# Kernel optimization log

Hardware: AMD Instinct MI355X
Metric: run time of the kernel (lower is better)

## Reference

```python
import jax, jax.numpy as jnp
import numpy as np

N, E, C, H, T, R = 32768, 262144, 128, 8, 8, 8
DK = C // H


def _typed_linear(feat, W, b, tid):
    # per-type linear: rows with tid==t get feat @ W[t] + b[t]; others untouched base 0
    out = jnp.zeros((feat.shape[0], W.shape[-1]), feat.dtype)
    for t in range(W.shape[0]):
        m = (tid == t)[:, None]
        out = jnp.where(m, feat @ W[t] + b[t], out)
    return out


def _forward(x, type_id, edge_index, edge_attr, Wk, bk, Wq, bq, Wv, bv, Wa, ba,
             relation_pri, relation_att, relation_msg, skip, gamma, beta):
    n, c = x.shape
    r, h, dk, _ = relation_att.shape
    src, dst = edge_index[0], edge_index[1]
    fs, fd = x[src], x[dst]                      # [E, C] gathers
    # per-edge-type k/q/v projections (source masks by edge_attr)
    k = _typed_linear(fs, Wk, bk, edge_attr).reshape(-1, h, dk)
    q = _typed_linear(fd, Wq, bq, edge_attr).reshape(-1, h, dk)
    v = _typed_linear(fs, Wv, bv, edge_attr).reshape(-1, h, dk)
    # relation transforms without materializing [E,h,dk,dk] gathers
    kt = jnp.zeros_like(k)
    vt = jnp.zeros_like(v)
    for ri in range(r):
        m = (edge_attr == ri)[:, None, None]
        kt = jnp.where(m, jnp.einsum('ehd,hdk->ehk', k, relation_att[ri]), kt)
        vt = jnp.where(m, jnp.einsum('ehd,hdk->ehk', v, relation_msg[ri]), vt)
    pri = relation_pri[edge_attr]                # [E, H]
    att = (q * kt).sum(-1) * pri / jnp.sqrt(jnp.asarray(dk, x.dtype))  # [E, H]
    # scatter softmax over destination-node groups
    mx = jax.ops.segment_max(att, dst, num_segments=n)
    ex = jnp.exp(att - mx[dst])
    den = jax.ops.segment_sum(ex, dst, num_segments=n)
    a = ex / den[dst]                            # [E, H]
    w = (a[..., None] * vt).reshape(-1, h * dk)  # [E, C]
    # scatter mean into node slots (zeros for isolated nodes)
    s = jax.ops.segment_sum(w, dst, num_segments=n)
    cnt = jax.ops.segment_sum(jnp.ones((w.shape[0], 1), x.dtype), dst, num_segments=n)
    x0 = jnp.where(cnt > 0, s / jnp.maximum(cnt, 1.0), 0.0)
    # per-node-type output projection + gated residual
    x0 = _typed_linear(x0, Wa, ba, type_id)
    alpha = jax.nn.sigmoid(skip)[type_id][:, None]
    out = x0 * alpha + x * (1.0 - alpha)
    # type-indexed LayerNorm (eps = 1e-5), dropout is identity in eval
    mu = out.mean(-1, keepdims=True)
    var = ((out - mu) ** 2).mean(-1, keepdims=True)
    xn = (out - mu) / jnp.sqrt(var + 1e-5)
    return xn * gamma[type_id] + beta[type_id]


def setup_inputs() -> dict:
    key = jax.random.key(0)
    ks = jax.random.split(key, 16)
    w = 1.0 / np.sqrt(C)
    wr = 1.0 / np.sqrt(DK)
    return {
        'x': jax.random.normal(ks[0], (N, C), jnp.float32),
        'type_id': jax.random.randint(ks[1], (N,), 0, T),
        'edge_index': jax.random.randint(ks[2], (2, E), 0, N),
        'edge_attr': jax.random.randint(ks[3], (E,), 0, R),
        'Wk': jax.random.normal(ks[4], (T, C, C), jnp.float32) * w,
        'bk': jax.random.normal(ks[5], (T, C), jnp.float32) * 0.02,
        'Wq': jax.random.normal(ks[6], (T, C, C), jnp.float32) * w,
        'bq': jax.random.normal(ks[7], (T, C), jnp.float32) * 0.02,
        'Wv': jax.random.normal(ks[8], (T, C, C), jnp.float32) * w,
        'bv': jax.random.normal(ks[9], (T, C), jnp.float32) * 0.02,
        'Wa': jax.random.normal(ks[10], (T, C, C), jnp.float32) * w,
        'ba': jax.random.normal(ks[11], (T, C), jnp.float32) * 0.02,
        'relation_pri': jnp.ones((R, H), jnp.float32),
        'relation_att': jax.random.normal(ks[12], (R, H, DK, DK), jnp.float32) * wr,
        'relation_msg': jax.random.normal(ks[13], (R, H, DK, DK), jnp.float32) * wr,
        'skip': jnp.ones((T,), jnp.float32),
        'gamma': jnp.ones((T, C), jnp.float32),
        'beta': jnp.zeros((T, C), jnp.float32),
    }


def reference(x, type_id, edge_index, edge_attr, Wk, bk, Wq, bq, Wv, bv, Wa, ba,
              relation_pri, relation_att, relation_msg, skip, gamma, beta):
    return _forward(x, type_id, edge_index, edge_attr, Wk, bk, Wq, bq, Wv, bv, Wa, ba,
                    relation_pri, relation_att, relation_msg, skip, gamma, beta)
```

## Files before the change

### kernel.cpp

```cpp
#include <hip/hip_runtime.h>
#include <math.h>

#define NN 32768
#define NE 262144
#define CD 128
#define NH 8
#define NT 8
#define NR 8

typedef unsigned short u16;
typedef unsigned long long ull;
typedef __attribute__((ext_vector_type(8))) short bhalf8;
typedef __attribute__((ext_vector_type(4))) float f32x4;


__device__ __forceinline__ u16 f2b(float f) {
    union { float f; unsigned u; } v; v.f = f;
    unsigned r = v.u + 0x7FFF + ((v.u >> 16) & 1);
    return (u16)(r >> 16);
}
__device__ __forceinline__ float b2f(unsigned h) {
    union { unsigned u; float f; } v; v.u = h << 16;
    return v.f;
}

#define PREP_BLOCKS 2057
#define XB_BLOCKS 2048
#define HIST_BLOCKS 1024

__global__ void prep_all(const float* __restrict__ Wk, const float* __restrict__ bk,
                         const float* __restrict__ Wq,
                         const float* __restrict__ Wv, const float* __restrict__ bv,
                         const float* __restrict__ Wa,
                         const float* __restrict__ Aatt, const float* __restrict__ Amsg,
                         const float* __restrict__ x,
                         const int* __restrict__ ea, const int* __restrict__ tidv,
                         const int* __restrict__ dstv,
                         u16* __restrict__ WqT, u16* __restrict__ WkT,
                         u16* __restrict__ WvT, u16* __restrict__ WaT,
                         float* __restrict__ bkf, float* __restrict__ bvf,
                         u16* __restrict__ xb,
                         int* __restrict__ epart, int* __restrict__ npart,
                         int* __restrict__ deg) {
    const int bx = blockIdx.x;
    if (bx >= PREP_BLOCKS + XB_BLOCKS) {
        __shared__ int wc[4][8];
        const int hb = bx - PREP_BLOCKS - XB_BLOCKS;
        const int tid = threadIdx.x;
        const int lane = tid & 63, w = tid >> 6;
        int i = hb * 256 + tid;
        int t = ea[i];
        atomicAdd(&deg[dstv[i]], 1);
#pragma unroll
        for (int u = 0; u < 8; ++u) {
            ull m = __ballot(t == u);
            if (lane == 0) wc[w][u] = __popcll(m);
        }
        __syncthreads();
        if (tid < 8) epart[hb * 8 + tid] = wc[0][tid] + wc[1][tid] + wc[2][tid] + wc[3][tid];
        if (hb < NN / 256) {
            int tn = tidv[i];
            __syncthreads();
#pragma unroll
            for (int u = 0; u < 8; ++u) {
                ull m = __ballot(tn == u);
                if (lane == 0) wc[w][u] = __popcll(m);
            }
            __syncthreads();
            if (tid < 8) npart[hb * 8 + tid] = wc[0][tid] + wc[1][tid] + wc[2][tid] + wc[3][tid];
        }
        return;
    }
    if (bx >= PREP_BLOCKS) {
        int zi = (bx - PREP_BLOCKS) * 256 + threadIdx.x;
        long basei = (long)zi * 8;
        float4 v0 = *(const float4*)(x + basei);
        float4 v1 = *(const float4*)(x + basei + 4);
        bhalf8 pk;
        pk[0] = (short)f2b(v0.x); pk[1] = (short)f2b(v0.y);
        pk[2] = (short)f2b(v0.z); pk[3] = (short)f2b(v0.w);
        pk[4] = (short)f2b(v1.x); pk[5] = (short)f2b(v1.y);
        pk[6] = (short)f2b(v1.z); pk[7] = (short)f2b(v1.w);
        *(bhalf8*)(xb + basei) = pk;
        return;
    }
    const int WCNT = NT * CD * CD;
    int idx = bx * 256 + threadIdx.x;
    if (idx < 4 * WCNT) {
        int mat = idx >> 17;
        int o = idx & (WCNT - 1);
        int t = o >> 14;
        int n = (o >> 7) & 127;
        int k = o & 127;
        int ct = n >> 4, lx2 = n & 15, kk = k >> 5, qd = (k >> 3) & 3, dd = k & 7;
        int oo = t * 16384 + (((ct * 4 + kk) * 4 + qd) * 16 + lx2) * 8 + dd;
        if (mat == 0) {
            WqT[oo] = f2b(Wq[(t * CD + k) * CD + n]);
        } else if (mat == 3) {
            WaT[oo] = f2b(Wa[(t * CD + k) * CD + n]);
        } else {
            int h = n >> 4, j = n & 15;
            const float* W = (mat == 1) ? Wk : Wv;
            const float* A = (mat == 1) ? Aatt : Amsg;
            const float* wrow = W + (t * CD + k) * CD + h * 16;
            const float* acol = A + ((t * NH + h) * 16) * 16 + j;
            float s = 0.f;
#pragma unroll
            for (int d = 0; d < 16; ++d) s += wrow[d] * acol[d * 16];
            ((mat == 1) ? WkT : WvT)[oo] = f2b(s);
        }
    } else {
        int o2 = idx - 4 * WCNT;
        if (o2 < 2 * NT * CD) {
            int which = (o2 >= NT * CD) ? 1 : 0;
            int o = o2 - which * NT * CD;
            const float* B = which ? bv : bk;
            const float* A = which ? Amsg : Aatt;
            int t = o >> 7; int c = o & 127; int h = c >> 4; int j = c & 15;
            const float* brow = B + t * CD + h * 16;
            const float* acol = A + ((t * NH + h) * 16) * 16 + j;
            float s = 0.f;
#pragma unroll
            for (int d = 0; d < 16; ++d) s += brow[d] * acol[d * 16];
            (which ? bvf : bkf)[o] = s;
        }
    }
}

__launch_bounds__(1024)
__global__ void scan_all(const int* __restrict__ deg, int* __restrict__ dbase,
                         int* __restrict__ epart, int* __restrict__ npart,
                         int* __restrict__ ectr, int* __restrict__ nctr) {
    const int t = threadIdx.x;
    if (blockIdx.x == 0) {
        __shared__ int part[1024];
        int local[32];
        int s = 0;
#pragma unroll
        for (int i = 0; i < 32; ++i) { local[i] = s; s += deg[t * 32 + i]; }
        part[t] = s;
        __syncthreads();
        for (int off = 1; off < 1024; off <<= 1) {
            int v = (t >= off) ? part[t - off] : 0;
            __syncthreads();
            part[t] += v;
            __syncthreads();
        }
        int base = (t == 0) ? 0 : part[t - 1];
#pragma unroll
        for (int i = 0; i < 32; ++i) dbase[t * 32 + i] = base + local[i];
        return;
    }
    __shared__ int sc[1024 * 8];
    int v[8], orig[8];
#pragma unroll
    for (int u = 0; u < 8; ++u) { orig[u] = v[u] = epart[t * 8 + u]; sc[t * 8 + u] = v[u]; }
    for (int off = 1; off < 1024; off <<= 1) {
        __syncthreads();
        int wv[8];
        bool p = (t >= off);
        if (p) {
#pragma unroll
            for (int u = 0; u < 8; ++u) wv[u] = sc[(t - off) * 8 + u];
        }
        __syncthreads();
        if (p) {
#pragma unroll
            for (int u = 0; u < 8; ++u) { v[u] += wv[u]; sc[t * 8 + u] = v[u]; }
        }
    }
    __syncthreads();
    int tot[8], base[8];
    {
        int acc = 0;
#pragma unroll
        for (int u = 0; u < 8; ++u) { tot[u] = sc[1023 * 8 + u]; base[u] = acc; acc += tot[u]; }
    }
#pragma unroll
    for (int u = 0; u < 8; ++u) epart[t * 8 + u] = base[u] + v[u] - orig[u];
    if (t == 0) {
        ectr[8] = 0; ectr[17] = 0;
        int acc = 0, ptb = 0;
        for (int u = 0; u < 8; ++u) {
            acc += tot[u]; ectr[9 + u] = acc;
            ptb += (tot[u] + 63) >> 6; ectr[18 + u] = ptb;
        }
    }
    __syncthreads();
    int nv[8], nor[8];
#pragma unroll
    for (int u = 0; u < 8; ++u) {
        nor[u] = nv[u] = (t < 128) ? npart[t * 8 + u] : 0;
        sc[t * 8 + u] = nv[u];
    }
    for (int off = 1; off < 128; off <<= 1) {
        __syncthreads();
        int wv[8];
        bool p = (t >= off && t < 128);
        if (p) {
#pragma unroll
            for (int u = 0; u < 8; ++u) wv[u] = sc[(t - off) * 8 + u];
        }
        __syncthreads();
        if (p) {
#pragma unroll
            for (int u = 0; u < 8; ++u) { nv[u] += wv[u]; sc[t * 8 + u] = nv[u]; }
        }
    }
    __syncthreads();
    int ntot[8], nbase[8];
    {
        int acc = 0;
#pragma unroll
        for (int u = 0; u < 8; ++u) { ntot[u] = sc[127 * 8 + u]; nbase[u] = acc; acc += ntot[u]; }
    }
    if (t < 128) {
#pragma unroll
        for (int u = 0; u < 8; ++u) npart[t * 8 + u] = nbase[u] + nv[u] - nor[u];
    }
    if (t == 0) {
        nctr[8] = 0; nctr[17] = 0;
        int acc = 0, ptb = 0;
        for (int u = 0; u < 8; ++u) {
            acc += ntot[u]; nctr[9 + u] = acc;
            ptb += (ntot[u] + 63) >> 6; nctr[18 + u] = ptb;
        }
    }
}

__global__ void scatter2(const int* __restrict__ ea, const int* __restrict__ tidv,
                         const int* __restrict__ srcv, const int* __restrict__ dstv,
                         const int* __restrict__ epart, const int* __restrict__ npart,
                         const int* __restrict__ dbase, int* __restrict__ dcur,
                         int4* __restrict__ epack, int* __restrict__ nperm) {
    __shared__ int wc[4][8];
    __shared__ int wo[4][8];
    const int b = blockIdx.x;
    const int tid = threadIdx.x;
    const int lane = tid & 63, w = tid >> 6;
    const bool is_e = (b < NE / 256);
    const int* lab; const int* off; int i;
    if (is_e) { lab = ea; off = epart + b * 8; i = b * 256 + tid; }
    else { lab = tidv; off = npart + (b - NE / 256) * 8; i = (b - NE / 256) * 256 + tid; }
    int t = lab[i];
    const ull below = (1ull << lane) - 1;
    int myrank = 0;
#pragma unroll
    for (int u = 0; u < 8; ++u) {
        ull m = __ballot(t == u);
        if (lane == 0) wc[w][u] = __popcll(m);
        if (t == u) myrank = __popcll(m & below);
    }
    __syncthreads();
    if (tid < 32) {
        int u = tid & 7, w2 = tid >> 3;
        int s = 0;
        for (int w3 = 0; w3 < w2; ++w3) s += wc[w3][u];
        wo[w2][u] = s;
    }
    __syncthreads();
    int slot = off[t] + wo[w][t] + myrank;
    if (is_e) {
        int s = srcv[i], d = dstv[i];
        int pos = dbase[d] + atomicAdd(&dcur[d], 1);
        epack[slot] = int4{s, d, pos, 0};
    } else {
        nperm[slot] = i;
    }
}

__device__ __forceinline__ void gemm64g(const u16* __restrict__ sA,
                                        const u16* __restrict__ gW,
                                        int rh, int ch, int lx, int quad, int lane,
                                        const float* __restrict__ biasRow,
                                        f32x4 acc[2][4]) {
#pragma unroll
    for (int nt = 0; nt < 4; ++nt) {
        float bv = biasRow[ch * 64 + nt * 16 + lx];
        acc[0][nt] = f32x4{bv, bv, bv, bv};
        acc[1][nt] = f32x4{bv, bv, bv, bv};
    }
    const int m0 = rh * 32 + lx;
    const u16* wbase = gW + (ch * 4) * 2048 + lane * 8;
    bhalf8 bb[2][4];
#pragma unroll
    for (int nt = 0; nt < 4; ++nt)
        bb[0][nt] = *(const bhalf8*)(wbase + nt * 2048);
#pragma unroll
    for (int kk = 0; kk < 4; ++kk) {
        if (kk < 3) {
#pragma unroll
            for (int nt = 0; nt < 4; ++nt)
                bb[(kk + 1) & 1][nt] = *(const bhalf8*)(wbase + nt * 2048 + (kk + 1) * 512);
        }
        const int ko = kk * 32 + quad * 8;
        bhalf8 a0 = *(const bhalf8*)&sA[m0 * 136 + ko];
        bhalf8 a1 = *(const bhalf8*)&sA[(m0 + 16) * 136 + ko];
#pragma unroll
        for (int nt = 0; nt < 4; ++nt) {
            acc[0][nt] = __builtin_amdgcn_mfma_f32_16x16x32_bf16(a0, bb[kk & 1][nt], acc[0][nt], 0, 0, 0);
            acc[1][nt] = __builtin_amdgcn_mfma_f32_16x16x32_bf16(a1, bb[kk & 1][nt], acc[1][nt], 0, 0, 0);
        }
    }
}

__launch_bounds__(256, 4)
__global__ void edge_kernel(const u16* __restrict__ xb,
                            const u16* __restrict__ WqT, const float* __restrict__ bq,
                            const u16* __restrict__ WkT, const float* __restrict__ bkf,
                            const u16* __restrict__ WvT, const float* __restrict__ bvf,
                            const float* __restrict__ pri,
                            const int* __restrict__ ectr, const int4* __restrict__ epack,
                            float* __restrict__ exs, u16* __restrict__ vts) {
    __shared__ u16 sFS[64 * 136];
    __shared__ u16 sFD[64 * 136];
    __shared__ int sSrc[64], sDst[64], sPos[64];

    const int tid = threadIdx.x;
    const int lane = tid & 63;
    const int w = tid >> 6;
    const int lx = lane & 15;
    const int quad = lane >> 4;
    const int ch = w & 1;
    const int rh = w >> 1;
    const int b = blockIdx.x;

    int t = -1, lt = 0;
#pragma unroll
    for (int u = 0; u < NR; ++u) {
        int p0 = ectr[17 + u], p1 = ectr[18 + u];
        if (b >= p0 && b < p1) { t = u; lt = b - p0; }
    }
    if (t < 0) return;
    const int base = ectr[8 + t];
    const int sz = ectr[9 + t] - base;
    const int start = lt * 64;

    if (tid < 64) {
        int idx = start + tid;
        int4 pk = (idx < sz) ? epack[base + idx] : int4{0, 0, NE, 0};
        sSrc[tid] = pk.x;
        sDst[tid] = pk.y;
        sPos[tid] = pk.z;
    }
    __syncthreads();

#pragma unroll
    for (int it = 0; it < 4; ++it) {
        int c = tid + it * 256;
        int row = c >> 4, off = (c & 15) * 8;
        *(bhalf8*)&sFS[row * 136 + off] = *(const bhalf8*)&xb[(long)sSrc[row] * CD + off];
        *(bhalf8*)&sFD[row * 136 + off] = *(const bhalf8*)&xb[(long)sDst[row] * CD + off];
    }
    __syncthreads();

    f32x4 qa[2][4], ka[2][4];
    gemm64g(sFD, WqT + t * 16384, rh, ch, lx, quad, lane, bq + t * CD, qa);
    gemm64g(sFS, WkT + t * 16384, rh, ch, lx, quad, lane, bkf + t * CD, ka);

    float ex[2][4][4];
#pragma unroll
    for (int nt = 0; nt < 4; ++nt) {
        const float ph = pri[t * NH + ch * 4 + nt] * 0.25f;
#pragma unroll
        for (int mt = 0; mt < 2; ++mt) {
#pragma unroll
            for (int reg = 0; reg < 4; ++reg) {
                float p = qa[mt][nt][reg] * ka[mt][nt][reg];
                p += __shfl_xor(p, 1);
                p += __shfl_xor(p, 2);
                p += __shfl_xor(p, 4);
                p += __shfl_xor(p, 8);
                ex[mt][nt][reg] = __expf(p * ph);
            }
        }
    }
    if (lx == 0) {
#pragma unroll
        for (int mt = 0; mt < 2; ++mt)
#pragma unroll
            for (int reg = 0; reg < 4; ++reg) {
                int erow = rh * 32 + mt * 16 + quad * 4 + reg;
                float4 e4 = {ex[mt][0][reg], ex[mt][1][reg], ex[mt][2][reg], ex[mt][3][reg]};
                *(float4*)(exs + (long)sPos[erow] * 8 + ch * 4) = e4;
            }
    }

    f32x4 va[2][4];
    gemm64g(sFS, WvT + t * 16384, rh, ch, lx, quad, lane, bvf + t * CD, va);
    __syncthreads();
#pragma unroll
    for (int mt = 0; mt < 2; ++mt)
#pragma unroll
        for (int reg = 0; reg < 4; ++reg) {
            int erow = rh * 32 + mt * 16 + quad * 4 + reg;
#pragma unroll
            for (int nt = 0; nt < 4; ++nt)
                sFD[erow * 136 + ch * 64 + nt * 16 + lx] = f2b(va[mt][nt][reg]);
        }
    __syncthreads();
#pragma unroll
    for (int it = 0; it < 4; ++it) {
        int c = tid + it * 256;
        int row = c >> 4, off = (c & 15) * 8;
        *(bhalf8*)&vts[(long)sPos[row] * 128 + off] = *(const bhalf8*)&sFD[row * 136 + off];
    }
}

__launch_bounds__(256, 4)
__global__ void node_kernel(const float* __restrict__ x,
                            const u16* __restrict__ WaT, const float* __restrict__ ba,
                            const float* __restrict__ skip, const float* __restrict__ gamma,
                            const float* __restrict__ beta,
                            const int* __restrict__ nctr, const int* __restrict__ nperm,
                            const int* __restrict__ dbase, const int* __restrict__ deg,
                            const float* __restrict__ exs, const u16* __restrict__ vts,
                            float* __restrict__ out) {
    __shared__ u16 sX0[64 * 136];
    __shared__ int sNode[64], sVal[64];

    const int tid = threadIdx.x;
    const int lane = tid & 63;
    const int w = tid >> 6;
    const int lx = lane & 15;
    const int quad = lane >> 4;
    const int b = blockIdx.x;

    int t = -1, lt = 0;
#pragma unroll
    for (int u = 0; u < NT; ++u) {
        int p0 = nctr[17 + u], p1 = nctr[18 + u];
        if (b >= p0 && b < p1) { t = u; lt = b - p0; }
    }
    if (t < 0) return;
    const int base = nctr[8 + t];
    const int sz = nctr[9 + t] - base;
    const int start = lt * 64;

    if (tid < 64) {
        int idx = start + tid;
        int n = (idx < sz) ? nperm[base + idx] : -1;
        sVal[tid] = (n >= 0) ? 1 : 0;
        sNode[tid] = (n >= 0) ? n : 0;
    }
    __syncthreads();

    {
        const int sub = lane >> 3;
        const int l8 = lane & 7;
        for (int r2 = 0; r2 < 2; ++r2) {
            int row = w * 16 + r2 * 8 + sub;
            int n = sNode[row];
            int s = dbase[n], d = deg[n];
            const u16* vp = vts + (long)s * 128 + l8 * 16;
            const float* ep = exs + (long)s * 8 + l8;
            float aA[16], aB[16];
#pragma unroll
            for (int c = 0; c < 16; ++c) { aA[c] = 0.f; aB[c] = 0.f; }
            float sdA = 0.f, sdB = 0.f;
            int j = 0;
            for (; j + 4 <= d; j += 4) {
                bhalf8 v0a = *(const bhalf8*)(vp + (long)(j + 0) * 128);
                bhalf8 v0b = *(const bhalf8*)(vp + (long)(j + 0) * 128 + 8);
                bhalf8 v1a = *(const bhalf8*)(vp + (long)(j + 1) * 128);
                bhalf8 v1b = *(const bhalf8*)(vp + (long)(j + 1) * 128 + 8);
                bhalf8 v2a = *(const bhalf8*)(vp + (long)(j + 2) * 128);
                bhalf8 v2b = *(const bhalf8*)(vp + (long)(j + 2) * 128 + 8);
                bhalf8 v3a = *(const bhalf8*)(vp + (long)(j + 3) * 128);
                bhalf8 v3b = *(const bhalf8*)(vp + (long)(j + 3) * 128 + 8);
                float e0 = ep[(long)(j + 0) * 8];
                float e1 = ep[(long)(j + 1) * 8];
                float e2 = ep[(long)(j + 2) * 8];
                float e3 = ep[(long)(j + 3) * 8];
#pragma unroll
                for (int c = 0; c < 8; ++c) {
                    aA[c] += e0 * b2f((u16)v0a[c]) + e1 * b2f((u16)v1a[c]);
                    aA[8 + c] += e0 * b2f((u16)v0b[c]) + e1 * b2f((u16)v1b[c]);
                    aB[c] += e2 * b2f((u16)v2a[c]) + e3 * b2f((u16)v3a[c]);
                    aB[8 + c] += e2 * b2f((u16)v2b[c]) + e3 * b2f((u16)v3b[c]);
                }
                sdA += e0 + e1;
                sdB += e2 + e3;
            }
            for (; j < d; ++j) {
                bhalf8 v0a = *(const bhalf8*)(vp + (long)j * 128);
                bhalf8 v0b = *(const bhalf8*)(vp + (long)j * 128 + 8);
                float e0 = ep[(long)j * 8];
#pragma unroll
                for (int c = 0; c < 8; ++c) {
                    aA[c] += e0 * b2f((u16)v0a[c]);
                    aA[8 + c] += e0 * b2f((u16)v0b[c]);
                }
                sdA += e0;
            }
            float sden = sdA + sdB;
            float inv = (d > 0) ? 1.f / (sden * (float)d) : 0.f;
            bhalf8 p0, p1;
#pragma unroll
            for (int c = 0; c < 8; ++c) {
                p0[c] = (short)f2b((aA[c] + aB[c]) * inv);
                p1[c] = (short)f2b((aA[8 + c] + aB[8 + c]) * inv);
            }
            *(bhalf8*)&sX0[row * 136 + l8 * 16] = p0;
            *(bhalf8*)&sX0[row * 136 + l8 * 16 + 8] = p1;
        }
    }
    __syncthreads();

    f32x4 acc[8];
#pragma unroll
    for (int nt = 0; nt < 8; ++nt) {
        float bv = ba[t * CD + nt * 16 + lx];
        acc[nt] = f32x4{bv, bv, bv, bv};
    }
    const int m0 = w * 16 + lx;
    const u16* wbase = WaT + t * 16384 + lane * 8;
#pragma unroll
    for (int kk = 0; kk < 4; ++kk) {
        bhalf8 nb[8];
#pragma unroll
        for (int ct = 0; ct < 8; ++ct)
            nb[ct] = *(const bhalf8*)(wbase + ct * 2048 + kk * 512);
        bhalf8 a = *(const bhalf8*)&sX0[m0 * 136 + kk * 32 + quad * 8];
#pragma unroll
        for (int ct = 0; ct < 8; ++ct)
            acc[ct] = __builtin_amdgcn_mfma_f32_16x16x32_bf16(a, nb[ct], acc[ct], 0, 0, 0);
    }

    const float alpha = 1.f / (1.f + __expf(-skip[t]));
    const float oma = 1.f - alpha;
    float g[8], be[8];
#pragma unroll
    for (int nt = 0; nt < 8; ++nt) {
        g[nt] = gamma[t * CD + nt * 16 + lx];
        be[nt] = beta[t * CD + nt * 16 + lx];
    }
#pragma unroll
    for (int reg = 0; reg < 4; ++reg) {
        int erow = w * 16 + quad * 4 + reg;
        int n = sNode[erow];
        const float* xr = x + (long)n * CD;
        float o[8];
        float s1 = 0.f, s2 = 0.f;
#pragma unroll
        for (int nt = 0; nt < 8; ++nt) {
            float xv = xr[nt * 16 + lx];
            float ov = acc[nt][reg] * alpha + xv * oma;
            o[nt] = ov;
            s1 += ov;
            s2 += ov * ov;
        }
#pragma unroll
        for (int m = 1; m < 16; m <<= 1) {
            s1 += __shfl_xor(s1, m);
            s2 += __shfl_xor(s2, m);
        }
        float mu = s1 * (1.f / 128.f);
        float var = s2 * (1.f / 128.f) - mu * mu;
        float rs = rsqrtf(var + 1e-5f);
        if (sVal[erow]) {
            float* op = out + (long)n * CD;
#pragma unroll
            for (int nt = 0; nt < 8; ++nt)
                __builtin_nontemporal_store((o[nt] - mu) * rs * g[nt] + be[nt],
                                            &op[nt * 16 + lx]);
        }
    }
}

extern "C" void kernel_launch(void* const* d_in, const int* in_sizes, int n_in,
                              void* d_out, int out_size, void* d_ws, size_t ws_size,
                              hipStream_t stream) {
    const float* x        = (const float*)d_in[0];
    const int*   type_id  = (const int*)d_in[1];
    const int*   edge_idx = (const int*)d_in[2];
    const int*   edge_attr= (const int*)d_in[3];
    const float* Wk   = (const float*)d_in[4];
    const float* bk   = (const float*)d_in[5];
    const float* Wq   = (const float*)d_in[6];
    const float* bq   = (const float*)d_in[7];
    const float* Wv   = (const float*)d_in[8];
    const float* bv   = (const float*)d_in[9];
    const float* Wa   = (const float*)d_in[10];
    const float* ba   = (const float*)d_in[11];
    const float* pri  = (const float*)d_in[12];
    const float* Aatt = (const float*)d_in[13];
    const float* Amsg = (const float*)d_in[14];
    const float* skip = (const float*)d_in[15];
    const float* gam  = (const float*)d_in[16];
    const float* bet  = (const float*)d_in[17];

    char* ws = (char*)d_ws;
    u16*   WqT  = (u16*)(ws + 0);
    u16*   WkT  = (u16*)(ws + 262144);
    u16*   WvT  = (u16*)(ws + 524288);
    u16*   WaT  = (u16*)(ws + 786432);
    float* bkf  = (float*)(ws + 1048576);
    float* bvf  = (float*)(ws + 1052672);
    float* exs  = (float*)(ws + 1056768);
    u16*   vts  = (u16*)(ws + 9447424);
    int*   deg  = (int*)  (ws + 76572672);
    int*   dcur = (int*)  (ws + 76703744);
    int*   dbase= (int*)  (ws + 76834816);
    int*   nperm= (int*)  (ws + 78014464);
    int*   ectr = (int*)  (ws + 78145536);
    int*   nctr = (int*)  (ws + 78145792);
    int*   epart= (int*)  (ws + 78146048);
    int*   npart= (int*)  (ws + 78178816);
    u16*   xb   = (u16*)  (ws + 78182912);
    int4*  epack= (int4*) (ws + 86571520);

    const int* src = edge_idx;
    const int* dst = edge_idx + NE;

    hipMemsetAsync(deg, 0, 2 * NN * sizeof(int), stream);
    prep_all<<<PREP_BLOCKS + XB_BLOCKS + HIST_BLOCKS, 256, 0, stream>>>(
        Wk, bk, Wq, Wv, bv, Wa, Aatt, Amsg, x, edge_attr, type_id, dst,
        WqT, WkT, WvT, WaT, bkf, bvf, xb, epart, npart, deg);
    scan_all<<<2, 1024, 0, stream>>>(deg, dbase, epart, npart, ectr, nctr);
    scatter2<<<NE / 256 + NN / 256, 256, 0, stream>>>(edge_attr, type_id, src, dst,
                                                      epart, npart, dbase, dcur,
                                                      epack, nperm);
    edge_kernel<<<NE / 64 + NR, 256, 0, stream>>>(xb, WqT, bq, WkT, bkf, WvT, bvf,
                                                  pri, ectr, epack, exs, vts);
    node_kernel<<<NN / 64 + NT, 256, 0, stream>>>(x, WaT, ba, skip, gam, bet, nctr, nperm,
                                                  dbase, deg, exs, vts, (float*)d_out);
}
```

Measured before the change: 240.8 us.

## Stream dst features directly into Q GEMM registers, drop sFD, use bf16 residual

The edge kernel no longer stages destination-node features in shared memory. The Q projection loads its A operands straight from global bf16 x with register double-buffering, and the V result reuses the sFS buffer. Halving the edge kernel's LDS footprint allows the launch-bounds occupancy hint to rise from 4 to 5 blocks. The node kernel also reads the residual x from the bf16 copy instead of fp32, which halves that traffic but lowers residual precision.

Result: slower. 306.7 us (+27.4%).

```diff
diff --git a/kernel.cpp b/kernel.cpp
--- a/kernel.cpp
+++ b/kernel.cpp
@@ -304,7 +304,7 @@
     }
 }
 
-__launch_bounds__(256, 4)
+__launch_bounds__(256, 5)
 __global__ void edge_kernel(const u16* __restrict__ xb,
                             const u16* __restrict__ WqT, const float* __restrict__ bq,
                             const u16* __restrict__ WkT, const float* __restrict__ bkf,
@@ -313,7 +313,6 @@
                             const int* __restrict__ ectr, const int4* __restrict__ epack,
                             float* __restrict__ exs, u16* __restrict__ vts) {
     __shared__ u16 sFS[64 * 136];
-    __shared__ u16 sFD[64 * 136];
     __shared__ int sSrc[64], sDst[64], sPos[64];
 
     const int tid = threadIdx.x;
@@ -350,12 +349,47 @@
         int c = tid + it * 256;
         int row = c >> 4, off = (c & 15) * 8;
         *(bhalf8*)&sFS[row * 136 + off] = *(const bhalf8*)&xb[(long)sSrc[row] * CD + off];
-        *(bhalf8*)&sFD[row * 136 + off] = *(const bhalf8*)&xb[(long)sDst[row] * CD + off];
-    }
-    __syncthreads();
-
-    f32x4 qa[2][4], ka[2][4];
-    gemm64g(sFD, WqT + t * 16384, rh, ch, lx, quad, lane, bq + t * CD, qa);
+    }
+
+    const int m0 = rh * 32 + lx;
+    const int aoff = quad * 8;
+
+    f32x4 qa[2][4];
+    {
+        const u16* pa0 = xb + (long)sDst[m0] * CD + aoff;
+        const u16* pa1 = xb + (long)sDst[m0 + 16] * CD + aoff;
+        const u16* wbase = WqT + t * 16384 + (ch * 4) * 2048 + lane * 8;
+#pragma unroll
+        for (int nt = 0; nt < 4; ++nt) {
+            float bv = bq[t * CD + ch * 64 + nt * 16 + lx];
+            qa[0][nt] = f32x4{bv, bv, bv, bv};
+            qa[1][nt] = f32x4{bv, bv, bv, bv};
+        }
+        bhalf8 aq0[2], aq1[2], bb[2][4];
+        aq0[0] = *(const bhalf8*)pa0;
+        aq1[0] = *(const bhalf8*)pa1;
+#pragma unroll
+        for (int nt = 0; nt < 4; ++nt)
+            bb[0][nt] = *(const bhalf8*)(wbase + nt * 2048);
+#pragma unroll
+        for (int kk = 0; kk < 4; ++kk) {
+            if (kk < 3) {
+                aq0[(kk + 1) & 1] = *(const bhalf8*)(pa0 + (kk + 1) * 32);
+                aq1[(kk + 1) & 1] = *(const bhalf8*)(pa1 + (kk + 1) * 32);
+#pragma unroll
+                for (int nt = 0; nt < 4; ++nt)
+                    bb[(kk + 1) & 1][nt] = *(const bhalf8*)(wbase + nt * 2048 + (kk + 1) * 512);
+            }
+#pragma unroll
+            for (int nt = 0; nt < 4; ++nt) {
+                qa[0][nt] = __builtin_amdgcn_mfma_f32_16x16x32_bf16(aq0[kk & 1], bb[kk & 1][nt], qa[0][nt], 0, 0, 0);
+                qa[1][nt] = __builtin_amdgcn_mfma_f32_16x16x32_bf16(aq1[kk & 1], bb[kk & 1][nt], qa[1][nt], 0, 0, 0);
+            }
+        }
+    }
+    __syncthreads();
+
+    f32x4 ka[2][4];
     gemm64g(sFS, WkT + t * 16384, rh, ch, lx, quad, lane, bkf + t * CD, ka);
 
     float ex[2][4][4];
@@ -396,19 +430,19 @@
             int erow = rh * 32 + mt * 16 + quad * 4 + reg;
 #pragma unroll
             for (int nt = 0; nt < 4; ++nt)
-                sFD[erow * 136 + ch * 64 + nt * 16 + lx] = f2b(va[mt][nt][reg]);
+                sFS[erow * 136 + ch * 64 + nt * 16 + lx] = f2b(va[mt][nt][reg]);
         }
     __syncthreads();
 #pragma unroll
     for (int it = 0; it < 4; ++it) {
         int c = tid + it * 256;
         int row = c >> 4, off = (c & 15) * 8;
-        *(bhalf8*)&vts[(long)sPos[row] * 128 + off] = *(const bhalf8*)&sFD[row * 136 + off];
+        *(bhalf8*)&vts[(long)sPos[row] * 128 + off] = *(const bhalf8*)&sFS[row * 136 + off];
     }
 }
 
 __launch_bounds__(256, 4)
-__global__ void node_kernel(const float* __restrict__ x,
+__global__ void node_kernel(const u16* __restrict__ xb,
                             const u16* __restrict__ WaT, const float* __restrict__ ba,
                             const float* __restrict__ skip, const float* __restrict__ gamma,
                             const float* __restrict__ beta,
@@ -539,12 +573,12 @@
     for (int reg = 0; reg < 4; ++reg) {
         int erow = w * 16 + quad * 4 + reg;
         int n = sNode[erow];
-        const float* xr = x + (long)n * CD;
+        const u16* xr = xb + (long)n * CD;
         float o[8];
         float s1 = 0.f, s2 = 0.f;
 #pragma unroll
         for (int nt = 0; nt < 8; ++nt) {
-            float xv = xr[nt * 16 + lx];
+            float xv = b2f(xr[nt * 16 + lx]);
             float ov = acc[nt][reg] * alpha + xv * oma;
             o[nt] = ov;
             s1 += ov;
@@ -623,6 +657,6 @@
                                                       epack, nperm);
     edge_kernel<<<NE / 64 + NR, 256, 0, stream>>>(xb, WqT, bq, WkT, bkf, WvT, bvf,
                                                   pri, ectr, epack, exs, vts);
-    node_kernel<<<NN / 64 + NT, 256, 0, stream>>>(x, WaT, ba, skip, gam, bet, nctr, nperm,
+    node_kernel<<<NN / 64 + NT, 256, 0, stream>>>(xb, WaT, ba, skip, gam, bet, nctr, nperm,
                                                   dbase, deg, exs, vts, (float*)d_out);
 }
```
